# Kernel tuning notes

Measured on AMD Instinct MI355X. Metric: run time of the kernel, lower is better.

Reference implementation:

```python
import jax, jax.numpy as jnp
import numpy as np

K = 3          # kernel size
STRIDE = 1
PAD = 1
DIL = 1
BN_EPS = 1e-5


def _conv2d(x, w, b, stride=STRIDE, pad=PAD):
    out = jax.lax.conv_general_dilated(
        x, w, (stride, stride), [(pad, pad), (pad, pad)],
        dimension_numbers=("NCHW", "OIHW", "NCHW"))
    return out + b[None, :, None, None]


def _bilinear_sample(x, py, px):
    """Zero-padded bilinear sampling. x: [B,C,H,W]; py,px: [B,Ho,Wo] float coords."""
    B, C, H, W = x.shape
    y0 = jnp.floor(py)
    x0 = jnp.floor(px)
    wy1 = py - y0
    wx1 = px - x0
    x_flat = x.reshape(B, C, H * W)

    def gather(yi, xi, wgt):
        valid = (yi >= 0) & (yi <= H - 1) & (xi >= 0) & (xi <= W - 1)
        yc = jnp.clip(yi, 0, H - 1).astype(jnp.int32)
        xc = jnp.clip(xi, 0, W - 1).astype(jnp.int32)
        idx = (yc * W + xc).reshape(B, 1, -1)                      # [B,1,Ho*Wo]
        v = jnp.take_along_axis(x_flat, idx, axis=2)               # [B,C,Ho*Wo]
        v = v.reshape(B, C, py.shape[1], py.shape[2])
        return v * (wgt * valid)[:, None]

    return (gather(y0,     x0,     (1 - wy1) * (1 - wx1)) +
            gather(y0,     x0 + 1, (1 - wy1) * wx1) +
            gather(y0 + 1, x0,     wy1 * (1 - wx1)) +
            gather(y0 + 1, x0 + 1, wy1 * wx1))


def _forward(x, off_w, off_b, dc_w, dc_b, bn_gamma, bn_beta, bn_mean, bn_var):
    B, C, H, W = x.shape
    K2 = K * K
    om = _conv2d(x, off_w, off_b)                 # [B, 3*K2, H, W]
    offset = om[:, :2 * K2]                       # interleaved (dy, dx) per tap
    mask = jax.nn.sigmoid(om[:, 2 * K2:])         # [B, K2, H, W]

    # output pixel -> top-left input coordinate of the receptive field
    base_y = (jnp.arange(H) * STRIDE - PAD)[:, None]   # [H,1]
    base_x = (jnp.arange(W) * STRIDE - PAD)[None, :]   # [1,W]

    out = jnp.zeros((B, dc_w.shape[0], H, W), dtype=x.dtype)
    for k in range(K2):
        kh, kw = k // K, k % K
        py = base_y + kh * DIL + offset[:, 2 * k]      # [B,H,W]
        px = base_x + kw * DIL + offset[:, 2 * k + 1]  # [B,H,W]
        samp = _bilinear_sample(x, py, px) * mask[:, k][:, None]
        out = out + jnp.einsum('oc,bchw->bohw', dc_w[:, :, kh, kw], samp)
    out = out + dc_b[None, :, None, None]

    # BatchNorm (inference: running stats) + ReLU
    scale = bn_gamma / jnp.sqrt(bn_var + BN_EPS)
    out = out * scale[None, :, None, None] + (bn_beta - bn_mean * scale)[None, :, None, None]
    return jax.nn.relu(out)


def setup_inputs() -> dict:
    key = jax.random.key(0)
    ks = jax.random.split(key, 8)
    B, Cin, Cout, H, W = 8, 256, 256, 64, 64
    K2 = K * K
    x = jax.random.normal(ks[0], (B, Cin, H, W), dtype=jnp.float32)
    # NOTE: original init zeros the offset conv; we use small random weights so
    # offsets/masks are nontrivial and the bilinear path is exercised.
    off_w = jax.random.normal(ks[1], (3 * K2, Cin, K, K), dtype=jnp.float32) * 0.01
    off_b = jax.random.normal(ks[2], (3 * K2,), dtype=jnp.float32) * 0.01
    dc_w = jax.random.normal(ks[3], (Cout, Cin, K, K), dtype=jnp.float32) / np.sqrt(Cin * K2)
    dc_b = jax.random.normal(ks[4], (Cout,), dtype=jnp.float32) * 0.01
    bn_gamma = jnp.ones((Cout,), dtype=jnp.float32)
    bn_beta = jnp.zeros((Cout,), dtype=jnp.float32)
    bn_mean = jax.random.normal(ks[5], (Cout,), dtype=jnp.float32) * 0.1
    bn_var = jax.random.uniform(ks[6], (Cout,), dtype=jnp.float32) * 0.5 + 0.5
    return {"x": x, "off_w": off_w, "off_b": off_b, "dc_w": dc_w, "dc_b": dc_b,
            "bn_gamma": bn_gamma, "bn_beta": bn_beta,
            "bn_mean": bn_mean, "bn_var": bn_var}


def reference(x, off_w, off_b, dc_w, dc_b, bn_gamma, bn_beta, bn_mean, bn_var):
    return _forward(x, off_w, off_b, dc_w, dc_b, bn_gamma, bn_beta, bn_mean, bn_var)
```

## Files before the change

kernel.cpp:

```cpp
#include <hip/hip_runtime.h>
#include <hip/hip_bf16.h>
#include <hip/hip_fp16.h>
#include <cstdint>
#include <cstddef>

#define HH 64
#define WW 64
#define CIN 256
#define COUT 256
#define NB 8
#define HW (HH * WW)
#define BN_EPS 1e-5f

typedef __attribute__((ext_vector_type(8))) short s16x8;
typedef __attribute__((ext_vector_type(8))) unsigned short u16x8;
typedef __attribute__((ext_vector_type(4))) float f32x4;
typedef __attribute__((ext_vector_type(2))) float f32x2;
typedef __attribute__((ext_vector_type(4))) unsigned int u32x4;

static __device__ __forceinline__ float bf2f(unsigned short u) {
  unsigned int v = ((unsigned int)u) << 16;
  return __builtin_bit_cast(float, v);
}
static __device__ __forceinline__ unsigned short f2bf(float f) {
  __hip_bfloat16 h = __float2bfloat16(f);
  return __builtin_bit_cast(unsigned short, h);
}

__global__ __launch_bounds__(256) void k_tr(const float* __restrict__ x,
                                            unsigned short* __restrict__ xbf) {
  __shared__ float tile[64][65];
  int bid = blockIdx.x;
  int b = bid & 7;
  int r = bid >> 3;
  int ct = r & 3;
  int st = r >> 2;
  int lane = threadIdx.x & 63;
  int grp = threadIdx.x >> 6;
  int c0 = ct * 64, s0 = st * 64;
  const float* xb = x + (size_t)b * CIN * HW;
#pragma unroll
  for (int i = 0; i < 16; ++i) {
    int row = grp * 16 + i;
    tile[row][lane] = xb[(size_t)(c0 + row) * HW + s0 + lane];
  }
  __syncthreads();
  unsigned short* xo = xbf + (size_t)b * HW * CIN;
#pragma unroll
  for (int i = 0; i < 16; ++i) {
    int row = grp * 16 + i;
    xo[(size_t)(s0 + row) * CIN + c0 + lane] = f2bf(tile[lane][row]);
  }
}

__global__ __launch_bounds__(256) void k_wt(const float* __restrict__ dc_w,
                                            unsigned short* __restrict__ Wf) {
  int idx = blockIdx.x * 256 + threadIdx.x;
  if (idx >= 9 * 8 * 16 * 64 * 8) return;
  int j = idx & 7;
  int lane = (idx >> 3) & 63;
  int tile = (idx >> 9) & 15;
  int ks = (idx >> 13) & 7;
  int k = idx >> 16;
  int o = tile * 16 + (lane & 15);
  int c = ks * 32 + (lane >> 4) * 8 + j;
  Wf[idx] = f2bf(dc_w[((size_t)o * CIN + c) * 9 + k]);
}

__global__ __launch_bounds__(256) void k_owt(const float* __restrict__ off_w,
                                             unsigned short* __restrict__ OWf) {
  int idx = blockIdx.x * 256 + threadIdx.x;
  if (idx >= 9 * 8 * 2 * 64 * 8) return;
  int j = idx & 7;
  int lane = (idx >> 3) & 63;
  int kot = (idx >> 9) & 1;
  int ks = (idx >> 10) & 7;
  int t = idx >> 13;
  int ko = kot * 16 + (lane & 15);
  int c = ks * 32 + (lane >> 4) * 8 + j;
  unsigned short v = 0;
  if (ko < 27) v = f2bf(off_w[((size_t)ko * CIN + c) * 9 + t]);
  OWf[idx] = v;
}

__global__ void k_bn(const float* __restrict__ g, const float* __restrict__ be,
                     const float* __restrict__ m, const float* __restrict__ va,
                     const float* __restrict__ db, float* __restrict__ sc,
                     float* __restrict__ bi) {
  int o = threadIdx.x;
  float s = g[o] * rsqrtf(va[o] + BN_EPS);
  sc[o] = s;
  bi[o] = be[o] + (db[o] - m[o]) * s;
}

__global__ __launch_bounds__(256, 4) void k_main(
    const unsigned short* __restrict__ xbf, const unsigned short* __restrict__ OWf,
    const float* __restrict__ off_b, const unsigned short* __restrict__ Wf,
    const float* __restrict__ bnsc, const float* __restrict__ bnbi,
    float* __restrict__ out) {
  int bid = blockIdx.x;
  int b = bid & 7;
  int r = bid >> 3;
  int h = r & 63;
  int q = r >> 6;
  int wq = q * 32;
  int tid = threadIdx.x;
  int lane = tid & 63;
  int wave = tid >> 6;
  int l15 = lane & 15, l4 = lane >> 4;

  __shared__ __align__(16) unsigned short ubuf[34 * 256];
  __shared__ float om_lds[27][32];
  __shared__ unsigned short pre_offS[9][32][4];
  __shared__ __half pre_wH[9][32][4];

  const unsigned short* xb = xbf + (size_t)b * HW * CIN;

  f32x4 acc_oc[2];
  acc_oc[0] = (f32x4){0.f, 0.f, 0.f, 0.f};
  acc_oc[1] = (f32x4){0.f, 0.f, 0.f, 0.f};
  int ptile = wave & 1;
  int gstart = wq - 1;

  for (int kh = 0; kh < 3; ++kh) {
    int y = h + kh - 1;
    if (y < 0 || y >= HH) continue;
    __syncthreads();
    const unsigned short* srow = xb + (size_t)y * WW * CIN;
    for (int e = tid; e < 34 * 32; e += 256) {
      int col = e >> 5;
      int ch = e & 31;
      int g = gstart + col;
      u16x8 v = {0, 0, 0, 0, 0, 0, 0, 0};
      if (g >= 0 && g < WW) v = *(const u16x8*)(srow + (size_t)g * CIN + ch * 8);
      *(u16x8*)&ubuf[col * 256 + ((ch ^ (col & 7)) * 8)] = v;
    }
    __syncthreads();
    if (wave < 2) {
#pragma unroll
      for (int kw = 0; kw < 3; ++kw) {
        int prow = ptile * 16 + l15 + kw;
        int rs = prow & 7;
        const unsigned short* Atap =
            OWf + ((size_t)(kh * 3 + kw) * 8) * 1024 + lane * 8;
#pragma unroll
        for (int ks = 0; ks < 8; ++ks) {
          s16x8 bfrag = *(const s16x8*)&ubuf[prow * 256 + (((ks * 4 + l4) ^ rs) * 8)];
#pragma unroll
          for (int kot = 0; kot < 2; ++kot) {
            s16x8 afrag = *(const s16x8*)(Atap + ks * 1024 + kot * 512);
            acc_oc[kot] = __builtin_amdgcn_mfma_f32_16x16x32_bf16(afrag, bfrag,
                                                                  acc_oc[kot], 0, 0, 0);
          }
        }
      }
    }
  }
  if (wave < 2) {
#pragma unroll
    for (int kot = 0; kot < 2; ++kot) {
#pragma unroll
      for (int j = 0; j < 4; ++j) {
        int ko = kot * 16 + l4 * 4 + j;
        if (ko < 27) om_lds[ko][ptile * 16 + l15] = acc_oc[kot][j];
      }
    }
  }
  __syncthreads();

  for (int item = tid; item < 9 * 32; item += 256) {
    int k = item >> 5;
    int wl = item & 31;
    int w = wq + wl;
    int kh = k / 3, kw = k % 3;
    float offy = om_lds[2 * k][wl] + off_b[2 * k];
    float offx = om_lds[2 * k + 1][wl] + off_b[2 * k + 1];
    float mk = om_lds[18 + k][wl] + off_b[18 + k];
    mk = 1.0f / (1.0f + expf(-mk));
    float py = (float)(h - 1 + kh) + offy;
    float px = (float)(w - 1 + kw) + offx;
    float fy0 = floorf(py), fx0 = floorf(px);
    float wy1 = py - fy0, wx1 = px - fx0;
    int y0 = (int)fy0, x0 = (int)fx0;
    int y1 = y0 + 1, x1 = x0 + 1;
    bool vy0 = (y0 >= 0) && (y0 <= HH - 1);
    bool vy1 = (y1 >= 0) && (y1 <= HH - 1);
    bool vx0 = (x0 >= 0) && (x0 <= WW - 1);
    bool vx1 = (x1 >= 0) && (x1 <= WW - 1);
    int y0c = min(max(y0, 0), HH - 1), y1c = min(max(y1, 0), HH - 1);
    int x0c = min(max(x0, 0), WW - 1), x1c = min(max(x1, 0), WW - 1);
    pre_wH[k][wl][0] =
        __float2half((1.f - wy1) * (1.f - wx1) * mk * ((vy0 && vx0) ? 1.f : 0.f));
    pre_wH[k][wl][1] = __float2half((1.f - wy1) * wx1 * mk * ((vy0 && vx1) ? 1.f : 0.f));
    pre_wH[k][wl][2] = __float2half(wy1 * (1.f - wx1) * mk * ((vy1 && vx0) ? 1.f : 0.f));
    pre_wH[k][wl][3] = __float2half(wy1 * wx1 * mk * ((vy1 && vx1) ? 1.f : 0.f));
    pre_offS[k][wl][0] = (unsigned short)(y0c * WW + x0c);
    pre_offS[k][wl][1] = (unsigned short)(y0c * WW + x1c);
    pre_offS[k][wl][2] = (unsigned short)(y1c * WW + x0c);
    pre_offS[k][wl][3] = (unsigned short)(y1c * WW + x1c);
  }
  __syncthreads();

  {
    int slot = ((bid >> 3) ^ (bid >> 8)) & 3;
    for (int i = 0; i < slot; ++i) __builtin_amdgcn_s_sleep(25);
  }

  unsigned short(*S)[256] = (unsigned short(*)[256])ubuf;
  f32x4 acc[4][2];
#pragma unroll
  for (int i = 0; i < 4; ++i)
#pragma unroll
    for (int j = 0; j < 2; ++j) acc[i][j] = (f32x4){0.f, 0.f, 0.f, 0.f};

  int o_base = wave * 64;
  int hv = lane >> 5;
  int chunk = lane & 31;

  for (int k = 0; k < 9; ++k) {
    __syncthreads();
    {
#pragma unroll
      for (int pp = 0; pp < 4; ++pp) {
        int pl = wave * 8 + pp * 2 + hv;
        int i0 = ((int)pre_offS[k][pl][0]) << 8;
        int i1 = ((int)pre_offS[k][pl][1]) << 8;
        int i2 = ((int)pre_offS[k][pl][2]) << 8;
        int i3 = ((int)pre_offS[k][pl][3]) << 8;
        float w0 = __half2float(pre_wH[k][pl][0]);
        float w1 = __half2float(pre_wH[k][pl][1]);
        float w2 = __half2float(pre_wH[k][pl][2]);
        float w3 = __half2float(pre_wH[k][pl][3]);
        u32x4 m0 = __builtin_bit_cast(u32x4, *(const u16x8*)(xb + i0 + chunk * 8));
        u32x4 m1 = __builtin_bit_cast(u32x4, *(const u16x8*)(xb + i1 + chunk * 8));
        u32x4 m2 = __builtin_bit_cast(u32x4, *(const u16x8*)(xb + i2 + chunk * 8));
        u32x4 m3 = __builtin_bit_cast(u32x4, *(const u16x8*)(xb + i3 + chunk * 8));
        f32x2 w0p = {w0, w0}, w1p = {w1, w1}, w2p = {w2, w2}, w3p = {w3, w3};
        u32x4 ro;
#pragma unroll
        for (int s = 0; s < 4; ++s) {
          f32x2 t0 = {bf2f((unsigned short)(m0[s] & 0xffffu)),
                      __builtin_bit_cast(float, m0[s] & 0xffff0000u)};
          f32x2 t1 = {bf2f((unsigned short)(m1[s] & 0xffffu)),
                      __builtin_bit_cast(float, m1[s] & 0xffff0000u)};
          f32x2 t2 = {bf2f((unsigned short)(m2[s] & 0xffffu)),
                      __builtin_bit_cast(float, m2[s] & 0xffff0000u)};
          f32x2 t3 = {bf2f((unsigned short)(m3[s] & 0xffffu)),
                      __builtin_bit_cast(float, m3[s] & 0xffff0000u)};
          f32x2 a2 = t0 * w0p;
          a2 = __builtin_elementwise_fma(t1, w1p, a2);
          a2 = __builtin_elementwise_fma(t2, w2p, a2);
          a2 = __builtin_elementwise_fma(t3, w3p, a2);
          unsigned int o;
          asm("v_cvt_pk_bf16_f32 %0, %1, %2" : "=v"(o) : "v"(a2[0]), "v"(a2[1]));
          ro[s] = o;
        }
        int phys = chunk ^ (pl & 7);
        *(u16x8*)&S[pl][phys * 8] = __builtin_bit_cast(u16x8, ro);
      }
    }
    __syncthreads();
    const unsigned short* Wa = Wf + (size_t)k * 65536 + (wave * 4) * 512 + lane * 8;
#pragma unroll
    for (int ks = 0; ks < 8; ++ks) {
      s16x8 a[4], bf[2];
#pragma unroll
      for (int ot = 0; ot < 4; ++ot)
        a[ot] = *(const s16x8*)(Wa + ks * 8192 + ot * 512);
#pragma unroll
      for (int pt = 0; pt < 2; ++pt) {
        int pl = pt * 16 + l15;
        int slot = (ks * 4 + l4) ^ (pl & 7);
        bf[pt] = *(const s16x8*)&S[pl][slot * 8];
      }
#pragma unroll
      for (int ot = 0; ot < 4; ++ot)
#pragma unroll
        for (int pt = 0; pt < 2; ++pt)
          acc[ot][pt] = __builtin_amdgcn_mfma_f32_16x16x32_bf16(a[ot], bf[pt],
                                                                acc[ot][pt], 0, 0, 0);
    }
  }

#pragma unroll
  for (int ot = 0; ot < 4; ++ot) {
#pragma unroll
    for (int j = 0; j < 4; ++j) {
      int o = o_base + ot * 16 + l4 * 4 + j;
      float sc = bnsc[o], bi = bnbi[o];
      float* ob = out + (((size_t)b * COUT + o) * HH + h) * WW + wq;
#pragma unroll
      for (int pt = 0; pt < 2; ++pt) {
        ob[pt * 16 + l15] = fmaxf(fmaf(acc[ot][pt][j], sc, bi), 0.f);
      }
    }
  }
}

extern "C" void kernel_launch(void* const* d_in, const int* in_sizes, int n_in,
                              void* d_out, int out_size, void* d_ws, size_t ws_size,
                              hipStream_t stream) {
  const float* x = (const float*)d_in[0];
  const float* off_w = (const float*)d_in[1];
  const float* off_b = (const float*)d_in[2];
  const float* dc_w = (const float*)d_in[3];
  const float* dc_b = (const float*)d_in[4];
  const float* bn_gamma = (const float*)d_in[5];
  const float* bn_beta = (const float*)d_in[6];
  const float* bn_mean = (const float*)d_in[7];
  const float* bn_var = (const float*)d_in[8];
  float* out = (float*)d_out;

  char* ws = (char*)d_ws;
  unsigned short* xbf = (unsigned short*)ws;
  ws += (size_t)NB * HW * CIN * sizeof(unsigned short);
  unsigned short* Wf = (unsigned short*)ws;
  ws += (size_t)9 * 8 * 16 * 64 * 8 * sizeof(unsigned short);
  unsigned short* OWf = (unsigned short*)ws;
  ws += (size_t)9 * 8 * 2 * 64 * 8 * sizeof(unsigned short);
  float* bnsc = (float*)ws;
  ws += 256 * sizeof(float);
  float* bnbi = (float*)ws;

  k_tr<<<NB * 64 * 4, 256, 0, stream>>>(x, xbf);
  k_wt<<<(9 * 8 * 16 * 64 * 8 + 255) / 256, 256, 0, stream>>>(dc_w, Wf);
  k_owt<<<(9 * 8 * 2 * 64 * 8 + 255) / 256, 256, 0, stream>>>(off_w, OWf);
  k_bn<<<1, 256, 0, stream>>>(bn_gamma, bn_beta, bn_mean, bn_var, dc_b, bnsc, bnbi);
  k_main<<<NB * HH * 2, 256, 0, stream>>>(xbf, OWf, off_b, Wf, bnsc, bnbi, out);
}
```

Baseline: 106.4 us.

## Prefetch gathers and weight fragments into registers before sampling and MFMA

Each tap iteration now issues all 16 bilinear gather loads and the first half of the weight fragments up front, then does the interpolation math. The second half of the weights loads after the barrier, ahead of the MFMA loop, and sched_barriers keep that ordering. This is meant to hide global memory latency behind compute. It also drops the staggered s_sleep start and a redundant barrier, and relaxes launch bounds from 4 to 2 blocks per SM so more registers are available. The trade-off is that higher register pressure can lower occupancy.

Result: slower. 112.5 us (+5.7%).

```diff
diff --git a/kernel.cpp b/kernel.cpp
--- a/kernel.cpp
+++ b/kernel.cpp
@@ -93,7 +93,7 @@
   bi[o] = be[o] + (db[o] - m[o]) * s;
 }
 
-__global__ __launch_bounds__(256, 4) void k_main(
+__global__ __launch_bounds__(256, 2) void k_main(
     const unsigned short* __restrict__ xbf, const unsigned short* __restrict__ OWf,
     const float* __restrict__ off_b, const unsigned short* __restrict__ Wf,
     const float* __restrict__ bnsc, const float* __restrict__ bnbi,
@@ -199,12 +199,6 @@
     pre_offS[k][wl][2] = (unsigned short)(y1c * WW + x0c);
     pre_offS[k][wl][3] = (unsigned short)(y1c * WW + x1c);
   }
-  __syncthreads();
-
-  {
-    int slot = ((bid >> 3) ^ (bid >> 8)) & 3;
-    for (int i = 0; i < slot; ++i) __builtin_amdgcn_s_sleep(25);
-  }
 
   unsigned short(*S)[256] = (unsigned short(*)[256])ubuf;
   f32x4 acc[4][2];
@@ -219,54 +213,68 @@
 
   for (int k = 0; k < 9; ++k) {
     __syncthreads();
-    {
-#pragma unroll
-      for (int pp = 0; pp < 4; ++pp) {
-        int pl = wave * 8 + pp * 2 + hv;
-        int i0 = ((int)pre_offS[k][pl][0]) << 8;
-        int i1 = ((int)pre_offS[k][pl][1]) << 8;
-        int i2 = ((int)pre_offS[k][pl][2]) << 8;
-        int i3 = ((int)pre_offS[k][pl][3]) << 8;
-        float w0 = __half2float(pre_wH[k][pl][0]);
-        float w1 = __half2float(pre_wH[k][pl][1]);
-        float w2 = __half2float(pre_wH[k][pl][2]);
-        float w3 = __half2float(pre_wH[k][pl][3]);
-        u32x4 m0 = __builtin_bit_cast(u32x4, *(const u16x8*)(xb + i0 + chunk * 8));
-        u32x4 m1 = __builtin_bit_cast(u32x4, *(const u16x8*)(xb + i1 + chunk * 8));
-        u32x4 m2 = __builtin_bit_cast(u32x4, *(const u16x8*)(xb + i2 + chunk * 8));
-        u32x4 m3 = __builtin_bit_cast(u32x4, *(const u16x8*)(xb + i3 + chunk * 8));
-        f32x2 w0p = {w0, w0}, w1p = {w1, w1}, w2p = {w2, w2}, w3p = {w3, w3};
-        u32x4 ro;
-#pragma unroll
-        for (int s = 0; s < 4; ++s) {
-          f32x2 t0 = {bf2f((unsigned short)(m0[s] & 0xffffu)),
-                      __builtin_bit_cast(float, m0[s] & 0xffff0000u)};
-          f32x2 t1 = {bf2f((unsigned short)(m1[s] & 0xffffu)),
-                      __builtin_bit_cast(float, m1[s] & 0xffff0000u)};
-          f32x2 t2 = {bf2f((unsigned short)(m2[s] & 0xffffu)),
-                      __builtin_bit_cast(float, m2[s] & 0xffff0000u)};
-          f32x2 t3 = {bf2f((unsigned short)(m3[s] & 0xffffu)),
-                      __builtin_bit_cast(float, m3[s] & 0xffff0000u)};
-          f32x2 a2 = t0 * w0p;
-          a2 = __builtin_elementwise_fma(t1, w1p, a2);
-          a2 = __builtin_elementwise_fma(t2, w2p, a2);
-          a2 = __builtin_elementwise_fma(t3, w3p, a2);
-          unsigned int o;
-          asm("v_cvt_pk_bf16_f32 %0, %1, %2" : "=v"(o) : "v"(a2[0]), "v"(a2[1]));
-          ro[s] = o;
-        }
-        int phys = chunk ^ (pl & 7);
-        *(u16x8*)&S[pl][phys * 8] = __builtin_bit_cast(u16x8, ro);
-      }
+    u16x8 g[4][4];
+#pragma unroll
+    for (int pp = 0; pp < 4; ++pp) {
+      int pl = wave * 8 + pp * 2 + hv;
+      g[pp][0] = *(const u16x8*)(xb + (((int)pre_offS[k][pl][0]) << 8) + chunk * 8);
+      g[pp][1] = *(const u16x8*)(xb + (((int)pre_offS[k][pl][1]) << 8) + chunk * 8);
+      g[pp][2] = *(const u16x8*)(xb + (((int)pre_offS[k][pl][2]) << 8) + chunk * 8);
+      g[pp][3] = *(const u16x8*)(xb + (((int)pre_offS[k][pl][3]) << 8) + chunk * 8);
+    }
+    const unsigned short* Wa = Wf + (size_t)k * 65536 + (wave * 4) * 512 + lane * 8;
+    s16x8 aRa[4][4];
+#pragma unroll
+    for (int ks = 0; ks < 4; ++ks)
+#pragma unroll
+      for (int ot = 0; ot < 4; ++ot)
+        aRa[ks][ot] = *(const s16x8*)(Wa + ks * 8192 + ot * 512);
+    __builtin_amdgcn_sched_barrier(0);
+#pragma unroll
+    for (int pp = 0; pp < 4; ++pp) {
+      int pl = wave * 8 + pp * 2 + hv;
+      float w0 = __half2float(pre_wH[k][pl][0]);
+      float w1 = __half2float(pre_wH[k][pl][1]);
+      float w2 = __half2float(pre_wH[k][pl][2]);
+      float w3 = __half2float(pre_wH[k][pl][3]);
+      u32x4 m0 = __builtin_bit_cast(u32x4, g[pp][0]);
+      u32x4 m1 = __builtin_bit_cast(u32x4, g[pp][1]);
+      u32x4 m2 = __builtin_bit_cast(u32x4, g[pp][2]);
+      u32x4 m3 = __builtin_bit_cast(u32x4, g[pp][3]);
+      f32x2 w0p = {w0, w0}, w1p = {w1, w1}, w2p = {w2, w2}, w3p = {w3, w3};
+      u32x4 ro;
+#pragma unroll
+      for (int s = 0; s < 4; ++s) {
+        f32x2 t0 = {bf2f((unsigned short)(m0[s] & 0xffffu)),
+                    __builtin_bit_cast(float, m0[s] & 0xffff0000u)};
+        f32x2 t1 = {bf2f((unsigned short)(m1[s] & 0xffffu)),
+                    __builtin_bit_cast(float, m1[s] & 0xffff0000u)};
+        f32x2 t2 = {bf2f((unsigned short)(m2[s] & 0xffffu)),
+                    __builtin_bit_cast(float, m2[s] & 0xffff0000u)};
+        f32x2 t3 = {bf2f((unsigned short)(m3[s] & 0xffffu)),
+                    __builtin_bit_cast(float, m3[s] & 0xffff0000u)};
+        f32x2 a2 = t0 * w0p;
+        a2 = __builtin_elementwise_fma(t1, w1p, a2);
+        a2 = __builtin_elementwise_fma(t2, w2p, a2);
+        a2 = __builtin_elementwise_fma(t3, w3p, a2);
+        unsigned int o;
+        asm("v_cvt_pk_bf16_f32 %0, %1, %2" : "=v"(o) : "v"(a2[0]), "v"(a2[1]));
+        ro[s] = o;
+      }
+      int phys = chunk ^ (pl & 7);
+      *(u16x8*)&S[pl][phys * 8] = __builtin_bit_cast(u16x8, ro);
     }
     __syncthreads();
-    const unsigned short* Wa = Wf + (size_t)k * 65536 + (wave * 4) * 512 + lane * 8;
-#pragma unroll
-    for (int ks = 0; ks < 8; ++ks) {
-      s16x8 a[4], bf[2];
+    s16x8 aRb[4][4];
+#pragma unroll
+    for (int ks = 0; ks < 4; ++ks)
 #pragma unroll
       for (int ot = 0; ot < 4; ++ot)
-        a[ot] = *(const s16x8*)(Wa + ks * 8192 + ot * 512);
+        aRb[ks][ot] = *(const s16x8*)(Wa + (ks + 4) * 8192 + ot * 512);
+    __builtin_amdgcn_sched_barrier(0);
+#pragma unroll
+    for (int ks = 0; ks < 4; ++ks) {
+      s16x8 bf[2];
 #pragma unroll
       for (int pt = 0; pt < 2; ++pt) {
         int pl = pt * 16 + l15;
@@ -277,7 +285,23 @@
       for (int ot = 0; ot < 4; ++ot)
 #pragma unroll
         for (int pt = 0; pt < 2; ++pt)
-          acc[ot][pt] = __builtin_amdgcn_mfma_f32_16x16x32_bf16(a[ot], bf[pt],
+          acc[ot][pt] = __builtin_amdgcn_mfma_f32_16x16x32_bf16(aRa[ks][ot], bf[pt],
+                                                                acc[ot][pt], 0, 0, 0);
+    }
+#pragma unroll
+    for (int ks = 0; ks < 4; ++ks) {
+      s16x8 bf[2];
+#pragma unroll
+      for (int pt = 0; pt < 2; ++pt) {
+        int pl = pt * 16 + l15;
+        int slot = ((ks + 4) * 4 + l4) ^ (pl & 7);
+        bf[pt] = *(const s16x8*)&S[pl][slot * 8];
+      }
+#pragma unroll
+      for (int ot = 0; ot < 4; ++ot)
+#pragma unroll
+        for (int pt = 0; pt < 2; ++pt)
+          acc[ot][pt] = __builtin_amdgcn_mfma_f32_16x16x32_bf16(aRb[ks][ot], bf[pt],
                                                                 acc[ot][pt], 0, 0, 0);
     }
   }
```

## Batch bilinear gathers across three taps with register double-buffering

Applied to the files above, without the earlier changes.

The main loop now handles the nine deformable taps in groups of three. For each group it issues global gathers for several taps ahead into two register buffers before combining them, then writes three sampled tiles into a tripled LDS buffer before running the MFMA GEMM over all three. This cuts the barrier count per tap and raises the number of gathers in flight to hide latency. It also drops the staggered s_sleep start and the barrier that came after the precompute, and lowers launch bounds to two blocks per CU. The cost is higher register and LDS pressure, which reduces occupancy.

Result: slower. 113.9 us (+7.0%).

```diff
diff --git a/kernel.cpp b/kernel.cpp
--- a/kernel.cpp
+++ b/kernel.cpp
@@ -93,7 +93,7 @@
   bi[o] = be[o] + (db[o] - m[o]) * s;
 }
 
-__global__ __launch_bounds__(256, 4) void k_main(
+__global__ __launch_bounds__(256, 2) void k_main(
     const unsigned short* __restrict__ xbf, const unsigned short* __restrict__ OWf,
     const float* __restrict__ off_b, const unsigned short* __restrict__ Wf,
     const float* __restrict__ bnsc, const float* __restrict__ bnbi,
@@ -109,7 +109,7 @@
   int wave = tid >> 6;
   int l15 = lane & 15, l4 = lane >> 4;
 
-  __shared__ __align__(16) unsigned short ubuf[34 * 256];
+  __shared__ __align__(16) unsigned short ubuf[3 * 32 * 256];
   __shared__ float om_lds[27][32];
   __shared__ unsigned short pre_offS[9][32][4];
   __shared__ __half pre_wH[9][32][4];
@@ -199,14 +199,8 @@
     pre_offS[k][wl][2] = (unsigned short)(y1c * WW + x0c);
     pre_offS[k][wl][3] = (unsigned short)(y1c * WW + x1c);
   }
-  __syncthreads();
-
-  {
-    int slot = ((bid >> 3) ^ (bid >> 8)) & 3;
-    for (int i = 0; i < slot; ++i) __builtin_amdgcn_s_sleep(25);
-  }
-
-  unsigned short(*S)[256] = (unsigned short(*)[256])ubuf;
+
+  unsigned short* S = ubuf;
   f32x4 acc[4][2];
 #pragma unroll
   for (int i = 0; i < 4; ++i)
@@ -217,68 +211,92 @@
   int hv = lane >> 5;
   int chunk = lane & 31;
 
-  for (int k = 0; k < 9; ++k) {
+  u16x8 gA[4][4], gB[4][4];
+
+  auto issue_into = [&](u16x8(&gg)[4][4], int kk) {
+#pragma unroll
+    for (int pp = 0; pp < 4; ++pp) {
+      int pl = wave * 8 + pp * 2 + hv;
+      gg[pp][0] = *(const u16x8*)(xb + (((int)pre_offS[kk][pl][0]) << 8) + chunk * 8);
+      gg[pp][1] = *(const u16x8*)(xb + (((int)pre_offS[kk][pl][1]) << 8) + chunk * 8);
+      gg[pp][2] = *(const u16x8*)(xb + (((int)pre_offS[kk][pl][2]) << 8) + chunk * 8);
+      gg[pp][3] = *(const u16x8*)(xb + (((int)pre_offS[kk][pl][3]) << 8) + chunk * 8);
+    }
+  };
+
+  auto combine_into = [&](u16x8(&gg)[4][4], int kk, int t) {
+#pragma unroll
+    for (int pp = 0; pp < 4; ++pp) {
+      int pl = wave * 8 + pp * 2 + hv;
+      float w0 = __half2float(pre_wH[kk][pl][0]);
+      float w1 = __half2float(pre_wH[kk][pl][1]);
+      float w2 = __half2float(pre_wH[kk][pl][2]);
+      float w3 = __half2float(pre_wH[kk][pl][3]);
+      u32x4 m0 = __builtin_bit_cast(u32x4, gg[pp][0]);
+      u32x4 m1 = __builtin_bit_cast(u32x4, gg[pp][1]);
+      u32x4 m2 = __builtin_bit_cast(u32x4, gg[pp][2]);
+      u32x4 m3 = __builtin_bit_cast(u32x4, gg[pp][3]);
+      f32x2 w0p = {w0, w0}, w1p = {w1, w1}, w2p = {w2, w2}, w3p = {w3, w3};
+      u32x4 ro;
+#pragma unroll
+      for (int s = 0; s < 4; ++s) {
+        f32x2 t0 = {bf2f((unsigned short)(m0[s] & 0xffffu)),
+                    __builtin_bit_cast(float, m0[s] & 0xffff0000u)};
+        f32x2 t1 = {bf2f((unsigned short)(m1[s] & 0xffffu)),
+                    __builtin_bit_cast(float, m1[s] & 0xffff0000u)};
+        f32x2 t2 = {bf2f((unsigned short)(m2[s] & 0xffffu)),
+                    __builtin_bit_cast(float, m2[s] & 0xffff0000u)};
+        f32x2 t3 = {bf2f((unsigned short)(m3[s] & 0xffffu)),
+                    __builtin_bit_cast(float, m3[s] & 0xffff0000u)};
+        f32x2 a2 = t0 * w0p;
+        a2 = __builtin_elementwise_fma(t1, w1p, a2);
+        a2 = __builtin_elementwise_fma(t2, w2p, a2);
+        a2 = __builtin_elementwise_fma(t3, w3p, a2);
+        unsigned int o;
+        asm("v_cvt_pk_bf16_f32 %0, %1, %2" : "=v"(o) : "v"(a2[0]), "v"(a2[1]));
+        ro[s] = o;
+      }
+      int phys = chunk ^ (pl & 7);
+      *(u16x8*)&S[t * 8192 + pl * 256 + phys * 8] = __builtin_bit_cast(u16x8, ro);
+    }
+  };
+
+  for (int grp = 0; grp < 3; ++grp) {
+    int k0 = grp * 3;
     __syncthreads();
-    {
-#pragma unroll
-      for (int pp = 0; pp < 4; ++pp) {
-        int pl = wave * 8 + pp * 2 + hv;
-        int i0 = ((int)pre_offS[k][pl][0]) << 8;
-        int i1 = ((int)pre_offS[k][pl][1]) << 8;
-        int i2 = ((int)pre_offS[k][pl][2]) << 8;
-        int i3 = ((int)pre_offS[k][pl][3]) << 8;
-        float w0 = __half2float(pre_wH[k][pl][0]);
-        float w1 = __half2float(pre_wH[k][pl][1]);
-        float w2 = __half2float(pre_wH[k][pl][2]);
-        float w3 = __half2float(pre_wH[k][pl][3]);
-        u32x4 m0 = __builtin_bit_cast(u32x4, *(const u16x8*)(xb + i0 + chunk * 8));
-        u32x4 m1 = __builtin_bit_cast(u32x4, *(const u16x8*)(xb + i1 + chunk * 8));
-        u32x4 m2 = __builtin_bit_cast(u32x4, *(const u16x8*)(xb + i2 + chunk * 8));
-        u32x4 m3 = __builtin_bit_cast(u32x4, *(const u16x8*)(xb + i3 + chunk * 8));
-        f32x2 w0p = {w0, w0}, w1p = {w1, w1}, w2p = {w2, w2}, w3p = {w3, w3};
-        u32x4 ro;
-#pragma unroll
-        for (int s = 0; s < 4; ++s) {
-          f32x2 t0 = {bf2f((unsigned short)(m0[s] & 0xffffu)),
-                      __builtin_bit_cast(float, m0[s] & 0xffff0000u)};
-          f32x2 t1 = {bf2f((unsigned short)(m1[s] & 0xffffu)),
-                      __builtin_bit_cast(float, m1[s] & 0xffff0000u)};
-          f32x2 t2 = {bf2f((unsigned short)(m2[s] & 0xffffu)),
-                      __builtin_bit_cast(float, m2[s] & 0xffff0000u)};
-          f32x2 t3 = {bf2f((unsigned short)(m3[s] & 0xffffu)),
-                      __builtin_bit_cast(float, m3[s] & 0xffff0000u)};
-          f32x2 a2 = t0 * w0p;
-          a2 = __builtin_elementwise_fma(t1, w1p, a2);
-          a2 = __builtin_elementwise_fma(t2, w2p, a2);
-          a2 = __builtin_elementwise_fma(t3, w3p, a2);
-          unsigned int o;
-          asm("v_cvt_pk_bf16_f32 %0, %1, %2" : "=v"(o) : "v"(a2[0]), "v"(a2[1]));
-          ro[s] = o;
+    issue_into(gA, k0);
+    issue_into(gB, k0 + 1);
+    __builtin_amdgcn_sched_barrier(0);
+    combine_into(gA, k0, 0);
+    issue_into(gA, k0 + 2);
+    __builtin_amdgcn_sched_barrier(0);
+    combine_into(gB, k0 + 1, 1);
+    combine_into(gA, k0 + 2, 2);
+    __syncthreads();
+#pragma unroll
+    for (int t = 0; t < 3; ++t) {
+      int k = k0 + t;
+      const unsigned short* Wa = Wf + (size_t)k * 65536 + (wave * 4) * 512 + lane * 8;
+      const unsigned short* St = S + t * 8192;
+#pragma unroll
+      for (int ks = 0; ks < 8; ++ks) {
+        s16x8 a[4], bf[2];
+#pragma unroll
+        for (int ot = 0; ot < 4; ++ot)
+          a[ot] = *(const s16x8*)(Wa + ks * 8192 + ot * 512);
+#pragma unroll
+        for (int pt = 0; pt < 2; ++pt) {
+          int pl = pt * 16 + l15;
+          int slot = (ks * 4 + l4) ^ (pl & 7);
+          bf[pt] = *(const s16x8*)(St + pl * 256 + slot * 8);
         }
-        int phys = chunk ^ (pl & 7);
-        *(u16x8*)&S[pl][phys * 8] = __builtin_bit_cast(u16x8, ro);
-      }
-    }
-    __syncthreads();
-    const unsigned short* Wa = Wf + (size_t)k * 65536 + (wave * 4) * 512 + lane * 8;
-#pragma unroll
-    for (int ks = 0; ks < 8; ++ks) {
-      s16x8 a[4], bf[2];
-#pragma unroll
-      for (int ot = 0; ot < 4; ++ot)
-        a[ot] = *(const s16x8*)(Wa + ks * 8192 + ot * 512);
-#pragma unroll
-      for (int pt = 0; pt < 2; ++pt) {
-        int pl = pt * 16 + l15;
-        int slot = (ks * 4 + l4) ^ (pl & 7);
-        bf[pt] = *(const s16x8*)&S[pl][slot * 8];
-      }
-#pragma unroll
-      for (int ot = 0; ot < 4; ++ot)
-#pragma unroll
-        for (int pt = 0; pt < 2; ++pt)
-          acc[ot][pt] = __builtin_amdgcn_mfma_f32_16x16x32_bf16(a[ot], bf[pt],
-                                                                acc[ot][pt], 0, 0, 0);
+#pragma unroll
+        for (int ot = 0; ot < 4; ++ot)
+#pragma unroll
+          for (int pt = 0; pt < 2; ++pt)
+            acc[ot][pt] = __builtin_amdgcn_mfma_f32_16x16x32_bf16(a[ot], bf[pt],
+                                                                  acc[ot][pt], 0, 0, 0);
+      }
     }
   }
 
```
